# Kernel optimization log

Measured on AMD Instinct MI355X. Metric: run time of the kernel, lower is better.

Reference implementation:

```python
import jax, jax.numpy as jnp
import numpy as np

N = 100000
E = 1600000
IN_DIM = 128
HID = 64
TDIM = 16
OUT_DIM = 2
NEG_SLOPE = 0.01  # F.leaky_relu default


def _linear_params(key, fan_in, fan_out):
    kw, kb = jax.random.split(key)
    s = 1.0 / np.sqrt(fan_in)
    w = jax.random.uniform(kw, (fan_in, fan_out), jnp.float32, -s, s)
    b = jax.random.uniform(kb, (fan_out,), jnp.float32, -s, s)
    return w, b


def setup_inputs() -> dict:
    key = jax.random.key(0)
    ks = jax.random.split(key, 12)
    x = jax.random.normal(ks[0], (N, IN_DIM), jnp.float32)
    edge_index = jax.random.randint(ks[1], (2, E), 0, N, jnp.int32)
    edge_time = jax.random.uniform(ks[2], (E, 1), jnp.float32)

    lin1_w, lin1_b = _linear_params(ks[3], IN_DIM, HID)
    attn1_w, attn1_b = _linear_params(ks[4], 2 * HID + TDIM, 1)
    t1_w, t1_b = _linear_params(ks[5], 1, TDIM)

    lin2_w, lin2_b = _linear_params(ks[6], HID, HID)
    attn2_w, attn2_b = _linear_params(ks[7], 2 * HID + TDIM, 1)
    t2_w, t2_b = _linear_params(ks[8], 1, TDIM)

    cls_w, cls_b = _linear_params(ks[9], HID, OUT_DIM)

    return dict(x=x, edge_index=edge_index, edge_time=edge_time,
                lin1_w=lin1_w, lin1_b=lin1_b, attn1_w=attn1_w, attn1_b=attn1_b,
                t1_w=t1_w, t1_b=t1_b,
                lin2_w=lin2_w, lin2_b=lin2_b, attn2_w=attn2_w, attn2_b=attn2_b,
                t2_w=t2_w, t2_b=t2_b, cls_w=cls_w, cls_b=cls_b)


def _segment_softmax(a, index, num_segments):
    # PyG softmax over variable-size neighborhoods grouped by destination node
    m = jax.ops.segment_max(a, index, num_segments=num_segments)
    e = jnp.exp(a - m[index])
    s = jax.ops.segment_sum(e, index, num_segments=num_segments)
    return e / (s[index] + 1e-16)


def _temporal_gat_conv(x, src, dst, edge_time,
                       lin_w, lin_b, attn_w, attn_b, t_w, t_b):
    # TemporalEncoding: sin(Linear(1, time_dim)(t))  -> [E, TDIM]
    t_enc = jnp.sin(edge_time @ t_w + t_b)
    # lin applied per-edge to x_i and x_j == lin applied once at node level then gathered
    h = x @ lin_w + lin_b                      # [N, HID]
    h_i = h[dst]                               # [E, HID] target features
    h_j = h[src]                               # [E, HID] source features
    alpha_in = jnp.concatenate([h_i, h_j, t_enc], axis=1)   # [E, 2*HID+TDIM]
    alpha = jax.nn.leaky_relu(alpha_in @ attn_w + attn_b, NEG_SLOPE)  # [E, 1]
    alpha = _segment_softmax(alpha, dst, x.shape[0])
    msg = h_j * alpha                          # [E, HID]
    return jax.ops.segment_sum(msg, dst, num_segments=x.shape[0])  # aggr='add'


def reference(x, edge_index, edge_time,
              lin1_w, lin1_b, attn1_w, attn1_b, t1_w, t1_b,
              lin2_w, lin2_b, attn2_w, attn2_b, t2_w, t2_b,
              cls_w, cls_b):
    src = edge_index[0]  # j (source)
    dst = edge_index[1]  # i (target / softmax segment index)
    h = _temporal_gat_conv(x, src, dst, edge_time,
                           lin1_w, lin1_b, attn1_w, attn1_b, t1_w, t1_b)
    h = jax.nn.relu(h)
    # dropout p=0.3 is identity in eval mode
    h = _temporal_gat_conv(h, src, dst, edge_time,
                           lin2_w, lin2_b, attn2_w, attn2_b, t2_w, t2_b)
    return h @ cls_w + cls_b  # [N, OUT_DIM]
```

## Files before the change

kernel.cpp:

```cpp
#include <hip/hip_runtime.h>

typedef unsigned short u16;
typedef unsigned int u32;

__device__ __forceinline__ float bf2f(u16 u) {
    return __uint_as_float(((u32)u) << 16);
}
__device__ __forceinline__ u16 f2bf(float f) {
    u32 u = __float_as_uint(f);
    u32 r = (u + 0x7fffu + ((u >> 16) & 1u)) >> 16;
    return (u16)r;
}
__device__ __forceinline__ float ldf(const void* p, int i, int isf32) {
    return isf32 ? ((const float*)p)[i] : bf2f(((const u16*)p)[i]);
}

#define P_W1   0
#define P_W2   8192
#define P_B1   12288
#define P_B2   12352
#define P_A1W  12416
#define P_A1B  12560
#define P_T1W  12561
#define P_T1B  12577
#define P_A2W  12593
#define P_A2B  12737
#define P_T2W  12738
#define P_T2B  12754
#define P_CLSW 12770
#define P_CLSB 12898
#define P_TOT  12900

#define CH   4096
#define NCHB 256
#define CAP  128

__global__ __launch_bounds__(256) void detect_dtype(
    const u32* __restrict__ xw, int nwords, int* __restrict__ flag)
{
    __shared__ int sbad;
    if (threadIdx.x == 0) sbad = 0;
    __syncthreads();
    int bad = 0;
    for (int i = threadIdx.x; i < nwords; i += 256) {
        u32 w = xw[i];
        int ea = (w >> 7) & 0xff;
        if (ea >= 0xF0) bad = 1;
    }
    if (bad) sbad = 1;
    __syncthreads();
    if (threadIdx.x == 0) flag[0] = sbad;
}

__global__ __launch_bounds__(256) void prep_params(
    const void* l1w, const void* l1b, const void* a1w, const void* a1b,
    const void* t1w, const void* t1b, const void* l2w, const void* l2b,
    const void* a2w, const void* a2b, const void* t2w, const void* t2b,
    const void* clsw, const void* clsb,
    const int* __restrict__ flag, float* __restrict__ P)
{
    const int f = flag[0];
    const int t = blockIdx.x * 256 + threadIdx.x;
    const int stride = gridDim.x * 256;
#define SEG(src, off, cnt) for (int i = t; i < (cnt); i += stride) P[(off) + i] = ldf(src, i, f)
    SEG(l1w, P_W1, 8192);
    SEG(l2w, P_W2, 4096);
    SEG(l1b, P_B1, 64);
    SEG(l2b, P_B2, 64);
    SEG(a1w, P_A1W, 144);
    SEG(a1b, P_A1B, 1);
    SEG(t1w, P_T1W, 16);
    SEG(t1b, P_T1B, 16);
    SEG(a2w, P_A2W, 144);
    SEG(a2b, P_A2B, 1);
    SEG(t2w, P_T2W, 16);
    SEG(t2b, P_T2B, 16);
    SEG(clsw, P_CLSW, 128);
    SEG(clsb, P_CLSB, 2);
#undef SEG
}

template<int K, int XMODE>
__global__ __launch_bounds__(256) void node_gemm(
    const void* __restrict__ xin, const float* __restrict__ P,
    int WOFF, int BOFF, int AOFF, const int* __restrict__ flag,
    u32* __restrict__ houtb, float* __restrict__ si, float* __restrict__ sj,
    int nnodes)
{
    __shared__ float Ws[K * 64];
    __shared__ float As[32][66];
    const int t = threadIdx.x;
    const int tx = t & 15;
    const int ty = t >> 4;
    const int base = blockIdx.x * 64;
    const bool xf32 = (XMODE == 0) ? (flag[0] != 0) : (XMODE == 1);

    for (int i = t * 4; i < K * 64; i += 1024)
        *(float4*)&Ws[i] = *(const float4*)&P[WOFF + i];

    float acc[4][4];
    #pragma unroll
    for (int r = 0; r < 4; ++r)
        #pragma unroll
        for (int c = 0; c < 4; ++c) acc[r][c] = 0.f;

    for (int k0 = 0; k0 < K; k0 += 32) {
        __syncthreads();
        if (xf32) {
            #pragma unroll
            for (int it = 0; it < 2; ++it) {
                int idx = t + it * 256;
                int row = idx >> 3, cq = (idx & 7) * 4;
                float4 v = make_float4(0.f, 0.f, 0.f, 0.f);
                if (base + row < nnodes)
                    v = *(const float4*)&((const float*)xin)[(size_t)(base + row) * K + k0 + cq];
                As[cq + 0][row] = v.x; As[cq + 1][row] = v.y;
                As[cq + 2][row] = v.z; As[cq + 3][row] = v.w;
            }
        } else {
            int row = t >> 2, q = (t & 3) * 8;
            uint4 v = make_uint4(0u, 0u, 0u, 0u);
            if (base + row < nnodes)
                v = *(const uint4*)&((const u16*)xin)[(size_t)(base + row) * K + k0 + q];
            As[q + 0][row] = bf2f((u16)(v.x & 0xffffu));
            As[q + 1][row] = bf2f((u16)(v.x >> 16));
            As[q + 2][row] = bf2f((u16)(v.y & 0xffffu));
            As[q + 3][row] = bf2f((u16)(v.y >> 16));
            As[q + 4][row] = bf2f((u16)(v.z & 0xffffu));
            As[q + 5][row] = bf2f((u16)(v.z >> 16));
            As[q + 6][row] = bf2f((u16)(v.w & 0xffffu));
            As[q + 7][row] = bf2f((u16)(v.w >> 16));
        }
        __syncthreads();

        #pragma unroll
        for (int k = 0; k < 32; ++k) {
            float2 a01 = *(float2*)&As[k][ty * 4];
            float2 a23 = *(float2*)&As[k][ty * 4 + 2];
            float4 b = *(float4*)&Ws[(k0 + k) * 64 + tx * 4];
            float a[4] = { a01.x, a01.y, a23.x, a23.y };
            float bb[4] = { b.x, b.y, b.z, b.w };
            #pragma unroll
            for (int r = 0; r < 4; ++r)
                #pragma unroll
                for (int c = 0; c < 4; ++c)
                    acc[r][c] = fmaf(a[r], bb[c], acc[r][c]);
        }
    }

    #pragma unroll
    for (int c = 0; c < 4; ++c) {
        float bc = P[BOFF + tx * 4 + c];
        #pragma unroll
        for (int r = 0; r < 4; ++r) acc[r][c] += bc;
    }

    float vi[4], vj[4];
    #pragma unroll
    for (int r = 0; r < 4; ++r) {
        float a_i = 0.f, a_j = 0.f;
        #pragma unroll
        for (int c = 0; c < 4; ++c) {
            a_i = fmaf(acc[r][c], P[AOFF + tx * 4 + c], a_i);
            a_j = fmaf(acc[r][c], P[AOFF + 64 + tx * 4 + c], a_j);
        }
        vi[r] = a_i; vj[r] = a_j;
    }
    #pragma unroll
    for (int o = 1; o < 16; o <<= 1) {
        #pragma unroll
        for (int r = 0; r < 4; ++r) {
            vi[r] += __shfl_xor(vi[r], o);
            vj[r] += __shfl_xor(vj[r], o);
        }
    }

    #pragma unroll
    for (int r = 0; r < 4; ++r) {
        int node = base + ty * 4 + r;
        if (node < nnodes) {
            u32 w0 = (u32)f2bf(acc[r][0]) | ((u32)f2bf(acc[r][1]) << 16);
            u32 w1 = (u32)f2bf(acc[r][2]) | ((u32)f2bf(acc[r][3]) << 16);
            *(uint2*)&houtb[(size_t)node * 32 + tx * 2] = make_uint2(w0, w1);
            if (tx == 0) { si[node] = vi[r]; sj[node] = vj[r]; }
        }
    }
}

__global__ __launch_bounds__(256) void count_chunks(
    const int* __restrict__ eid, int* __restrict__ chunkhist, int E)
{
    __shared__ int hist[NCHB];
    const int t = threadIdx.x, c = blockIdx.x;
    hist[t] = 0;
    __syncthreads();
    const int base = c * CH;
    #pragma unroll
    for (int i = 0; i < CH / 256; ++i) {
        int e = base + t + i * 256;
        if (e < E) atomicAdd(&hist[eid[e] >> 9], 1);
    }
    __syncthreads();
    chunkhist[c * NCHB + t] = hist[t];
}

__global__ __launch_bounds__(256) void scan_chunks(
    int* __restrict__ chunkhist, int* __restrict__ buckettot, int nchunks)
{
    __shared__ int s[512];
    const int b = blockIdx.x, t = threadIdx.x;
    int v0 = (t < nchunks) ? chunkhist[(size_t)t * NCHB + b] : 0;
    int v1 = (t + 256 < nchunks) ? chunkhist[(size_t)(t + 256) * NCHB + b] : 0;
    s[t] = v0; s[t + 256] = v1;
    __syncthreads();
    for (int off = 1; off < 512; off <<= 1) {
        int x0 = (t >= off) ? s[t - off] : 0;
        int x1 = s[t + 256 - off];
        __syncthreads();
        s[t] += x0; s[t + 256] += x1;
        __syncthreads();
    }
    if (t < nchunks) chunkhist[(size_t)t * NCHB + b] = s[t] - v0;
    if (t + 256 < nchunks) chunkhist[(size_t)(t + 256) * NCHB + b] = s[t + 256] - v1;
    if (t == 255) buckettot[b] = s[511];
}

__global__ __launch_bounds__(256) void bucket_start_scan(
    const int* __restrict__ buckettot, int* __restrict__ bucketstart,
    int* __restrict__ offs, int N)
{
    __shared__ int s[NCHB];
    const int b = threadIdx.x;
    int v = buckettot[b];
    s[b] = v;
    __syncthreads();
    for (int off = 1; off < NCHB; off <<= 1) {
        int x = (b >= off) ? s[b - off] : 0;
        __syncthreads();
        s[b] += x;
        __syncthreads();
    }
    bucketstart[b] = s[b] - v;
    if (b == NCHB - 1) { bucketstart[NCHB] = s[b]; offs[N] = s[b]; }
}

__global__ __launch_bounds__(256) void place_chunks(
    const int* __restrict__ ei, const void* __restrict__ et,
    const int* __restrict__ flag, const int* __restrict__ chunkhist,
    const int* __restrict__ bucketstart, int2* __restrict__ staging, int E)
{
    __shared__ int2 sorted[CH];
    __shared__ unsigned char bno[CH];
    __shared__ int hist[NCHB], lstart[NCHB], cur[NCHB], gb[NCHB];
    const int t = threadIdx.x, c = blockIdx.x;
    const int base = c * CH;
    const int f = flag[0];
    hist[t] = 0;
    gb[t] = bucketstart[t] + chunkhist[c * NCHB + t];
    __syncthreads();
    #pragma unroll
    for (int i = 0; i < CH / 256; ++i) {
        int e = base + t + i * 256;
        if (e < E) atomicAdd(&hist[ei[E + e] >> 9], 1);
    }
    __syncthreads();
    int v = hist[t];
    lstart[t] = v;
    __syncthreads();
    for (int off = 1; off < NCHB; off <<= 1) {
        int x = (t >= off) ? lstart[t - off] : 0;
        __syncthreads();
        lstart[t] += x;
        __syncthreads();
    }
    int ex = lstart[t] - v;
    __syncthreads();
    lstart[t] = ex;
    cur[t] = ex;
    __syncthreads();
    #pragma unroll
    for (int i = 0; i < CH / 256; ++i) {
        int e = base + t + i * 256;
        if (e < E) {
            int s_ = ei[e], d = ei[E + e];
            float tt = ldf(et, e, f);
            int b = d >> 9;
            int p = atomicAdd(&cur[b], 1);
            sorted[p] = make_int2(s_ | ((d & 511) << 17), __float_as_int(tt));
            bno[p] = (unsigned char)b;
        }
    }
    __syncthreads();
    const int cnt_tot = min(CH, E - base);
    for (int idx = t; idx < cnt_tot; idx += 256) {
        int b = bno[idx];
        staging[gb[b] + (idx - lstart[b])] = sorted[idx];
    }
}

__global__ __launch_bounds__(256) void bin_edges(
    const int2* __restrict__ staging, const int* __restrict__ bucketstart,
    int* __restrict__ offs, int2* __restrict__ csrA, int N)
{
    __shared__ int cnt[512], loc[512];
    const int b = blockIdx.x, t = threadIdx.x;
    const int beg = bucketstart[b], end = bucketstart[b + 1];
    const int nstart = b << 9;
    cnt[t] = 0; cnt[t + 256] = 0;
    __syncthreads();
    for (int i = beg + t; i < end; i += 256)
        atomicAdd(&cnt[(((u32)staging[i].x) >> 17) & 511], 1);
    __syncthreads();
    int v0 = cnt[t], v1 = cnt[t + 256];
    loc[t] = v0; loc[t + 256] = v1;
    __syncthreads();
    for (int off = 1; off < 512; off <<= 1) {
        int x0 = (t >= off) ? loc[t - off] : 0;
        int x1 = loc[t + 256 - off];
        __syncthreads();
        loc[t] += x0; loc[t + 256] += x1;
        __syncthreads();
    }
    int cur0 = beg + loc[t] - v0;
    int cur1 = beg + loc[t + 256] - v1;
    if (nstart + t < N) offs[nstart + t] = cur0;
    if (nstart + t + 256 < N) offs[nstart + t + 256] = cur1;
    cnt[t] = cur0; cnt[t + 256] = cur1;
    __syncthreads();
    for (int i = beg + t; i < end; i += 256) {
        int2 e = staging[i];
        int slot = atomicAdd(&cnt[(((u32)e.x) >> 17) & 511], 1);
        csrA[slot] = make_int2(e.x & 0x1ffff, e.y);
    }
}

__global__ __launch_bounds__(256) void temporal_pass(
    int2* __restrict__ csrA, int2* __restrict__ csrB,
    const float* __restrict__ P, int E)
{
    int i = blockIdx.x * 256 + threadIdx.x;
    if (i >= E) return;
    int2 e = csrA[i];
    float tt = __int_as_float(e.y);
    float td1 = P[P_A1B], td2 = P[P_A2B];
    #pragma unroll
    for (int k = 0; k < 16; ++k) {
        td1 += __sinf(fmaf(tt, P[P_T1W + k], P[P_T1B + k])) * P[P_A1W + 128 + k];
        td2 += __sinf(fmaf(tt, P[P_T2W + k], P[P_T2B + k])) * P[P_A2W + 128 + k];
    }
    csrA[i] = make_int2(e.x, __float_as_int(td1));
    csrB[i] = make_int2(e.x, __float_as_int(td2));
}

template<int MODE>
__global__ __launch_bounds__(256) void aggregate(
    const int* __restrict__ offs, const int2* __restrict__ csr2,
    const u32* __restrict__ hb,
    const float* __restrict__ si, const float* __restrict__ sjv,
    const float* __restrict__ P,
    u32* __restrict__ houtb, void* __restrict__ outp,
    const int* __restrict__ flag, int n)
{
    __shared__ int2 cache[4][2][CAP];
    const int wave = threadIdx.x >> 6;
    const int lane = threadIdx.x & 63;
    const int half = lane >> 5;
    const int hl = lane & 31;
    const int node = blockIdx.x * 8 + wave * 2 + half;
    const bool active = node < n;
    int beg = 0, end = 0;
    if (active) { beg = offs[node]; end = offs[node + 1]; }
    const int deg = end - beg;
    int2* cw = cache[wave][half];
    const float sii = active ? si[node] : 0.f;

    float ssum = 0.f;
    for (int idx = hl; idx < deg; idx += 32) {
        int2 st = csr2[beg + idx];
        float a = sii + sjv[st.x] + __int_as_float(st.y);
        a = (a > 0.f) ? a : 0.01f * a;
        float e = __expf(fminf(a, 80.f));
        if (idx < CAP) cw[idx] = make_int2(st.x, __float_as_int(e));
        ssum += e;
    }
    #pragma unroll
    for (int o = 16; o > 0; o >>= 1) ssum += __shfl_xor(ssum, o);

    const int degc = min(deg, CAP);
    const int degpad = (degc + 3) & ~3;
    if (hl < degpad - degc) cw[degc + hl] = make_int2(0, 0);

    float ax = 0.f, ay = 0.f;
    for (int j0 = 0; j0 < degpad; j0 += 4) {
        int2 s0 = cw[j0 + 0];
        int2 s1 = cw[j0 + 1];
        int2 s2 = cw[j0 + 2];
        int2 s3 = cw[j0 + 3];
        u32 p0 = hb[s0.x * 32 + hl];
        u32 p1 = hb[s1.x * 32 + hl];
        u32 p2 = hb[s2.x * 32 + hl];
        u32 p3 = hb[s3.x * 32 + hl];
        float e0 = __int_as_float(s0.y);
        float e1 = __int_as_float(s1.y);
        float e2 = __int_as_float(s2.y);
        float e3 = __int_as_float(s3.y);
        ax = fmaf(e0, __uint_as_float(p0 << 16), ax);
        ay = fmaf(e0, __uint_as_float(p0 & 0xffff0000u), ay);
        ax = fmaf(e1, __uint_as_float(p1 << 16), ax);
        ay = fmaf(e1, __uint_as_float(p1 & 0xffff0000u), ay);
        ax = fmaf(e2, __uint_as_float(p2 << 16), ax);
        ay = fmaf(e2, __uint_as_float(p2 & 0xffff0000u), ay);
        ax = fmaf(e3, __uint_as_float(p3 << 16), ax);
        ay = fmaf(e3, __uint_as_float(p3 & 0xffff0000u), ay);
    }
    for (int j = CAP; j < deg; ++j) {
        int2 st = csr2[beg + j];
        float a = sii + sjv[st.x] + __int_as_float(st.y);
        a = (a > 0.f) ? a : 0.01f * a;
        float e = __expf(fminf(a, 80.f));
        u32 pk = hb[st.x * 32 + hl];
        ax = fmaf(e, __uint_as_float(pk << 16), ax);
        ay = fmaf(e, __uint_as_float(pk & 0xffff0000u), ay);
    }

    if (!active) return;
    float inv = 1.0f / (ssum + 1e-16f);

    if (MODE == 0) {
        float r0 = fmaxf(ax * inv, 0.f);
        float r1 = fmaxf(ay * inv, 0.f);
        houtb[node * 32 + hl] = (u32)f2bf(r0) | ((u32)f2bf(r1) << 16);
    } else {
        float r0 = ax * inv, r1 = ay * inv;
        float l0 = r0 * P[P_CLSW + 4 * hl]     + r1 * P[P_CLSW + 4 * hl + 2];
        float l1 = r0 * P[P_CLSW + 4 * hl + 1] + r1 * P[P_CLSW + 4 * hl + 3];
        #pragma unroll
        for (int o = 16; o > 0; o >>= 1) {
            l0 += __shfl_xor(l0, o);
            l1 += __shfl_xor(l1, o);
        }
        if (hl == 0) {
            l0 += P[P_CLSB];
            l1 += P[P_CLSB + 1];
            if (flag[0]) {
                ((float2*)outp)[node] = make_float2(l0, l1);
            } else {
                ((u32*)outp)[node] = (u32)f2bf(l0) | ((u32)f2bf(l1) << 16);
            }
        }
    }
}

extern "C" void kernel_launch(void* const* d_in, const int* in_sizes, int n_in,
                              void* d_out, int out_size, void* d_ws, size_t ws_size,
                              hipStream_t stream)
{
    const void* x    = d_in[0];
    const int*  ei   = (const int*)d_in[1];
    const void* et   = d_in[2];
    const void* l1w  = d_in[3];
    const void* l1b  = d_in[4];
    const void* a1w  = d_in[5];
    const void* a1b  = d_in[6];
    const void* t1w  = d_in[7];
    const void* t1b  = d_in[8];
    const void* l2w  = d_in[9];
    const void* l2b  = d_in[10];
    const void* a2w  = d_in[11];
    const void* a2b  = d_in[12];
    const void* t2w  = d_in[13];
    const void* t2b  = d_in[14];
    const void* clsw = d_in[15];
    const void* clsb = d_in[16];

    const int N = in_sizes[0] / 128;
    const int E = in_sizes[2];
    const int nchunks = (E + CH - 1) / CH;
    const int nbkt = (N + 511) >> 9;

    char* ws = (char*)d_ws;
    size_t off = 0;
    auto A = [&](size_t bytes) -> char* {
        char* p = ws + off;
        off = (off + bytes + 255) & ~(size_t)255;
        return p;
    };
    int*   flag        = (int*)A(256);
    float* P           = (float*)A(P_TOT * 4);
    u32*   h1b         = (u32*)A((size_t)N * 32 * 4);
    float* si1         = (float*)A((size_t)N * 4);
    float* sj1         = (float*)A((size_t)N * 4);
    float* si2         = (float*)A((size_t)N * 4);
    float* sj2         = (float*)A((size_t)N * 4);
    int*   chunkhist   = (int*)A((size_t)nchunks * NCHB * 4);
    int*   buckettot   = (int*)A(NCHB * 4);
    int*   bucketstart = (int*)A((size_t)(NCHB + 1) * 4);
    int*   offs        = (int*)A((size_t)(N + 1) * 4);
    int2*  csrA        = (int2*)A((size_t)E * 8);
    int2*  csrB        = (int2*)A((size_t)E * 8);
    char*  unionr      = A((size_t)E * 8 < (size_t)N * 32 * 4
                           ? (size_t)N * 32 * 4 : (size_t)E * 8);
    int2*  staging     = (int2*)unionr;
    u32*   hagb        = (u32*)unionr;
    (void)ws_size; (void)n_in; (void)out_size;

    detect_dtype<<<1, 256, 0, stream>>>((const u32*)x, 4096, flag);

    prep_params<<<32, 256, 0, stream>>>(l1w, l1b, a1w, a1b, t1w, t1b,
                                        l2w, l2b, a2w, a2b, t2w, t2b,
                                        clsw, clsb, flag, P);

    node_gemm<128, 0><<<(N + 63) / 64, 256, 0, stream>>>(
        x, P, P_W1, P_B1, P_A1W, flag, h1b, si1, sj1, N);

    count_chunks<<<nchunks, 256, 0, stream>>>(ei + E, chunkhist, E);

    scan_chunks<<<NCHB, 256, 0, stream>>>(chunkhist, buckettot, nchunks);

    bucket_start_scan<<<1, 256, 0, stream>>>(buckettot, bucketstart, offs, N);

    place_chunks<<<nchunks, 256, 0, stream>>>(ei, et, flag, chunkhist,
                                              bucketstart, staging, E);

    bin_edges<<<nbkt, 256, 0, stream>>>(staging, bucketstart, offs, csrA, N);

    temporal_pass<<<(E + 255) / 256, 256, 0, stream>>>(csrA, csrB, P, E);

    aggregate<0><<<(N + 7) / 8, 256, 0, stream>>>(
        offs, csrA, h1b, si1, sj1, P, hagb, nullptr, flag, N);

    node_gemm<64, 2><<<(N + 63) / 64, 256, 0, stream>>>(
        hagb, P, P_W2, P_B2, P_A2W, flag, h1b, si2, sj2, N);

    aggregate<1><<<(N + 7) / 8, 256, 0, stream>>>(
        offs, csrB, h1b, si2, sj2, P, nullptr, d_out, flag, N);
}
```

Measured before the change: 325.1 us.

## Replace FMA node GEMMs with bf16 MFMA using split hi/lo weight fragments

Swaps the shared-memory FP32 FMA tiled node GEMM for a matrix-core version built on the 16x16x32 bf16 MFMA. A new prep kernel pre-swizzles the weights into per-lane fragment layout, split into high and low bf16 parts. FP32 inputs are also split, so three MFMAs per tile approximate FP32 precision. This removes LDS staging and barriers, but adds an extra launch, strided 2-byte output stores, and some precision loss versus true FP32.

```diff
diff --git a/kernel.cpp b/kernel.cpp
--- a/kernel.cpp
+++ b/kernel.cpp
@@ -2,6 +2,9 @@
 
 typedef unsigned short u16;
 typedef unsigned int u32;
+
+typedef __attribute__((ext_vector_type(8))) short short8v;
+typedef __attribute__((ext_vector_type(4))) float float4v;
 
 __device__ __forceinline__ float bf2f(u16 u) {
     return __uint_as_float(((u32)u) << 16);
@@ -34,6 +37,9 @@
 #define CH   4096
 #define NCHB 256
 #define CAP  128
+
+#define W1F_ELEMS 16384
+#define W2F_ELEMS 8192
 
 __global__ __launch_bounds__(256) void detect_dtype(
     const u32* __restrict__ xw, int nwords, int* __restrict__ flag)
@@ -80,109 +86,109 @@
 #undef SEG
 }
 
+__global__ __launch_bounds__(256) void prep_wfrags(
+    const float* __restrict__ P,
+    u16* __restrict__ w1h, u16* __restrict__ w1l,
+    u16* __restrict__ w2h, u16* __restrict__ w2l)
+{
+    int e = blockIdx.x * 256 + threadIdx.x;
+    if (e >= W1F_ELEMS + W2F_ELEMS) return;
+    int idx, woff;
+    u16 *dh, *dl;
+    if (e < W1F_ELEMS) { idx = e; woff = P_W1; dh = w1h; dl = w1l; }
+    else { idx = e - W1F_ELEMS; woff = P_W2; dh = w2h; dl = w2l; }
+    int j = idx & 7;
+    int l = (idx >> 3) & 63;
+    int ctks = idx >> 9;
+    int ct = ctks & 3;
+    int ks = ctks >> 2;
+    int k = ks * 32 + (l >> 4) * 8 + j;
+    int col = ct * 16 + (l & 15);
+    float wv = P[woff + k * 64 + col];
+    u16 hh = f2bf(wv);
+    dh[idx] = hh;
+    dl[idx] = f2bf(wv - bf2f(hh));
+}
+
 template<int K, int XMODE>
-__global__ __launch_bounds__(256) void node_gemm(
+__global__ __launch_bounds__(256) void node_gemm_mfma(
     const void* __restrict__ xin, const float* __restrict__ P,
-    int WOFF, int BOFF, int AOFF, const int* __restrict__ flag,
+    int BOFF, int AOFF, const int* __restrict__ flag,
+    const u16* __restrict__ wfh, const u16* __restrict__ wfl,
     u32* __restrict__ houtb, float* __restrict__ si, float* __restrict__ sj,
     int nnodes)
 {
-    __shared__ float Ws[K * 64];
-    __shared__ float As[32][66];
-    const int t = threadIdx.x;
-    const int tx = t & 15;
-    const int ty = t >> 4;
-    const int base = blockIdx.x * 64;
-    const bool xf32 = (XMODE == 0) ? (flag[0] != 0) : (XMODE == 1);
-
-    for (int i = t * 4; i < K * 64; i += 1024)
-        *(float4*)&Ws[i] = *(const float4*)&P[WOFF + i];
-
-    float acc[4][4];
-    #pragma unroll
-    for (int r = 0; r < 4; ++r)
+    const int l = threadIdx.x & 63;
+    const int w = threadIdx.x >> 6;
+    const int cl = l & 15;
+    const int cg = l >> 4;
+    const int rowbase = blockIdx.x * 64 + w * 16;
+    const bool xf32 = (XMODE == 0) ? (flag[0] != 0) : false;
+
+    const int arow = rowbase + cl;
+    const int arc = (arow < nnodes) ? arow : 0;
+    const int kb = cg * 8;
+
+    const u16* xb = (const u16*)xin;
+    const float* xf = (const float*)xin;
+    const short8v* bhp = (const short8v*)wfh;
+    const short8v* blp = (const short8v*)wfl;
+
+    float4v acc[4];
+    #pragma unroll
+    for (int ct = 0; ct < 4; ++ct) acc[ct] = (float4v){0.f, 0.f, 0.f, 0.f};
+
+    #pragma unroll
+    for (int ks = 0; ks < K / 32; ++ks) {
+        short8v ah, al_;
+        bool hasl = false;
+        if (XMODE == 2 || !xf32) {
+            ah = *(const short8v*)&xb[(size_t)arc * K + ks * 32 + kb];
+            al_ = (short8v){0, 0, 0, 0, 0, 0, 0, 0};
+        } else {
+            float4 v0 = *(const float4*)&xf[(size_t)arc * K + ks * 32 + kb];
+            float4 v1 = *(const float4*)&xf[(size_t)arc * K + ks * 32 + kb + 4];
+            float fv[8] = { v0.x, v0.y, v0.z, v0.w, v1.x, v1.y, v1.z, v1.w };
+            #pragma unroll
+            for (int j = 0; j < 8; ++j) {
+                u16 hh = f2bf(fv[j]);
+                ah[j] = (short)hh;
+                al_[j] = (short)f2bf(fv[j] - bf2f(hh));
+            }
+            hasl = true;
+        }
         #pragma unroll
-        for (int c = 0; c < 4; ++c) acc[r][c] = 0.f;
-
-    for (int k0 = 0; k0 < K; k0 += 32) {
-        __syncthreads();
-        if (xf32) {
-            #pragma unroll
-            for (int it = 0; it < 2; ++it) {
-                int idx = t + it * 256;
-                int row = idx >> 3, cq = (idx & 7) * 4;
-                float4 v = make_float4(0.f, 0.f, 0.f, 0.f);
-                if (base + row < nnodes)
-                    v = *(const float4*)&((const float*)xin)[(size_t)(base + row) * K + k0 + cq];
-                As[cq + 0][row] = v.x; As[cq + 1][row] = v.y;
-                As[cq + 2][row] = v.z; As[cq + 3][row] = v.w;
-            }
-        } else {
-            int row = t >> 2, q = (t & 3) * 8;
-            uint4 v = make_uint4(0u, 0u, 0u, 0u);
-            if (base + row < nnodes)
-                v = *(const uint4*)&((const u16*)xin)[(size_t)(base + row) * K + k0 + q];
-            As[q + 0][row] = bf2f((u16)(v.x & 0xffffu));
-            As[q + 1][row] = bf2f((u16)(v.x >> 16));
-            As[q + 2][row] = bf2f((u16)(v.y & 0xffffu));
-            As[q + 3][row] = bf2f((u16)(v.y >> 16));
-            As[q + 4][row] = bf2f((u16)(v.z & 0xffffu));
-            As[q + 5][row] = bf2f((u16)(v.z >> 16));
-            As[q + 6][row] = bf2f((u16)(v.w & 0xffffu));
-            As[q + 7][row] = bf2f((u16)(v.w >> 16));
-        }
-        __syncthreads();
-
+        for (int ct = 0; ct < 4; ++ct) {
+            short8v bh = bhp[(ks * 4 + ct) * 64 + l];
+            short8v bl = blp[(ks * 4 + ct) * 64 + l];
+            acc[ct] = __builtin_amdgcn_mfma_f32_16x16x32_bf16(ah, bh, acc[ct], 0, 0, 0);
+            acc[ct] = __builtin_amdgcn_mfma_f32_16x16x32_bf16(ah, bl, acc[ct], 0, 0, 0);
+            if (hasl)
+                acc[ct] = __builtin_amdgcn_mfma_f32_16x16x32_bf16(al_, bh, acc[ct], 0, 0, 0);
+        }
+    }
+
+    #pragma unroll
+    for (int r = 0; r < 4; ++r) {
+        int node = rowbase + cg * 4 + r;
+        float aiv = 0.f, ajv = 0.f;
+        u16 hs[4];
         #pragma unroll
-        for (int k = 0; k < 32; ++k) {
-            float2 a01 = *(float2*)&As[k][ty * 4];
-            float2 a23 = *(float2*)&As[k][ty * 4 + 2];
-            float4 b = *(float4*)&Ws[(k0 + k) * 64 + tx * 4];
-            float a[4] = { a01.x, a01.y, a23.x, a23.y };
-            float bb[4] = { b.x, b.y, b.z, b.w };
-            #pragma unroll
-            for (int r = 0; r < 4; ++r)
-                #pragma unroll
-                for (int c = 0; c < 4; ++c)
-                    acc[r][c] = fmaf(a[r], bb[c], acc[r][c]);
-        }
-    }
-
-    #pragma unroll
-    for (int c = 0; c < 4; ++c) {
-        float bc = P[BOFF + tx * 4 + c];
+        for (int ct = 0; ct < 4; ++ct) {
+            float v = acc[ct][r] + P[BOFF + ct * 16 + cl];
+            aiv = fmaf(v, P[AOFF + ct * 16 + cl], aiv);
+            ajv = fmaf(v, P[AOFF + 64 + ct * 16 + cl], ajv);
+            hs[ct] = f2bf(v);
+        }
         #pragma unroll
-        for (int r = 0; r < 4; ++r) acc[r][c] += bc;
-    }
-
-    float vi[4], vj[4];
-    #pragma unroll
-    for (int r = 0; r < 4; ++r) {
-        float a_i = 0.f, a_j = 0.f;
-        #pragma unroll
-        for (int c = 0; c < 4; ++c) {
-            a_i = fmaf(acc[r][c], P[AOFF + tx * 4 + c], a_i);
-            a_j = fmaf(acc[r][c], P[AOFF + 64 + tx * 4 + c], a_j);
-        }
-        vi[r] = a_i; vj[r] = a_j;
-    }
-    #pragma unroll
-    for (int o = 1; o < 16; o <<= 1) {
-        #pragma unroll
-        for (int r = 0; r < 4; ++r) {
-            vi[r] += __shfl_xor(vi[r], o);
-            vj[r] += __shfl_xor(vj[r], o);
-        }
-    }
-
-    #pragma unroll
-    for (int r = 0; r < 4; ++r) {
-        int node = base + ty * 4 + r;
+        for (int o = 1; o < 16; o <<= 1) {
+            aiv += __shfl_xor(aiv, o);
+            ajv += __shfl_xor(ajv, o);
+        }
         if (node < nnodes) {
-            u32 w0 = (u32)f2bf(acc[r][0]) | ((u32)f2bf(acc[r][1]) << 16);
-            u32 w1 = (u32)f2bf(acc[r][2]) | ((u32)f2bf(acc[r][3]) << 16);
-            *(uint2*)&houtb[(size_t)node * 32 + tx * 2] = make_uint2(w0, w1);
-            if (tx == 0) { si[node] = vi[r]; sj[node] = vj[r]; }
+            u16* hp = (u16*)houtb + (size_t)node * 64 + cl;
+            hp[0] = hs[0]; hp[16] = hs[1]; hp[32] = hs[2]; hp[48] = hs[3];
+            if (cl == 0) { si[node] = aiv; sj[node] = ajv; }
         }
     }
 }
@@ -487,6 +493,10 @@
     };
     int*   flag        = (int*)A(256);
     float* P           = (float*)A(P_TOT * 4);
+    u16*   w1fh        = (u16*)A(W1F_ELEMS * 2);
+    u16*   w1fl        = (u16*)A(W1F_ELEMS * 2);
+    u16*   w2fh        = (u16*)A(W2F_ELEMS * 2);
+    u16*   w2fl        = (u16*)A(W2F_ELEMS * 2);
     u32*   h1b         = (u32*)A((size_t)N * 32 * 4);
     float* si1         = (float*)A((size_t)N * 4);
     float* sj1         = (float*)A((size_t)N * 4);
@@ -510,8 +520,11 @@
                                         l2w, l2b, a2w, a2b, t2w, t2b,
                                         clsw, clsb, flag, P);
 
-    node_gemm<128, 0><<<(N + 63) / 64, 256, 0, stream>>>(
-        x, P, P_W1, P_B1, P_A1W, flag, h1b, si1, sj1, N);
+    prep_wfrags<<<(W1F_ELEMS + W2F_ELEMS) / 256, 256, 0, stream>>>(
+        P, w1fh, w1fl, w2fh, w2fl);
+
+    node_gemm_mfma<128, 0><<<(N + 63) / 64, 256, 0, stream>>>(
+        x, P, P_B1, P_A1W, flag, w1fh, w1fl, h1b, si1, sj1, N);
 
     count_chunks<<<nchunks, 256, 0, stream>>>(ei + E, chunkhist, E);
 
@@ -529,8 +542,8 @@
     aggregate<0><<<(N + 7) / 8, 256, 0, stream>>>(
         offs, csrA, h1b, si1, sj1, P, hagb, nullptr, flag, N);
 
-    node_gemm<64, 2><<<(N + 63) / 64, 256, 0, stream>>>(
-        hagb, P, P_W2, P_B2, P_A2W, flag, h1b, si2, sj2, N);
+    node_gemm_mfma<64, 2><<<(N + 63) / 64, 256, 0, stream>>>(
+        hagb, P, P_B2, P_A2W, flag, w2fh, w2fl, h1b, si2, sj2, N);
 
     aggregate<1><<<(N + 7) / 8, 256, 0, stream>>>(
         offs, csrB, h1b, si2, sj2, P, nullptr, d_out, flag, N);
```

New measurement: 299.7 us. 1.08x faster.
